# Performance work log

Hardware: AMD Instinct MI355X
Metric: run time of the kernel (lower is better)

The kernel has to match this reference:

```python
import jax, jax.numpy as jnp
import numpy as np

B, N, D, H = 4, 4096, 256, 8
HD = D // H
EPS = 1e-09


def _feature_map(t):
    # ELU(x) + 1, strictly positive feature map (Katharopoulos et al. 2020)
    return jax.nn.elu(t) + 1.0


def setup_inputs() -> dict:
    key = jax.random.key(0)
    ks = jax.random.split(key, 8)
    s = 0.02  # weight init scale for numerical stability
    return {
        "x": jax.random.normal(ks[0], (B, N, D), dtype=jnp.float32),
        "prior": jax.random.normal(ks[1], (B, N, N), dtype=jnp.float32),
        "Wq": jax.random.normal(ks[2], (D, D), dtype=jnp.float32) * s,
        "Wk": jax.random.normal(ks[3], (D, D), dtype=jnp.float32) * s,
        "Wv": jax.random.normal(ks[4], (D, D), dtype=jnp.float32) * s,
        "bv": jax.random.normal(ks[5], (D,), dtype=jnp.float32) * s,
        "Wo": jax.random.normal(ks[6], (D, D), dtype=jnp.float32) * s,
        "bo": jax.random.normal(ks[7], (D,), dtype=jnp.float32) * s,
    }


def reference(x, prior, Wq, Wk, Wv, bv, Wo, bo):
    b, n, d = x.shape
    # bias: mean over last axis of prior -> (b, n, 1, 1), broadcast over heads/dims
    bias = jnp.mean(prior, axis=-1)[:, :, None, None]
    q = _feature_map(jnp.einsum("bnd,ed->bne", x, Wq).reshape(b, n, H, HD) + bias)
    padding_mask = jnp.all(q == 0, axis=-1)  # (b, n, H)
    k = _feature_map(jnp.einsum("bnd,ed->bne", x, Wk).reshape(b, n, H, HD))
    v = _feature_map((jnp.einsum("bnd,ed->bne", x, Wv) + bv).reshape(b, n, H, HD))
    # KV summary state: (b, h, m, d) with m = value dim, d = key feature dim
    kv = jnp.einsum("bnhd,bnhm->bhmd", k, v)
    # normalizer: q . sum_n(k)
    z = 1.0 / (jnp.einsum("bnhd,bhd->bnh", q, jnp.sum(k, axis=1)) + EPS)
    attn = jnp.einsum("bnhd,bhmd,bnh->bnhm", q, kv, z)
    attn = jnp.where(padding_mask[..., None], 0.0, attn)
    attn = attn.reshape(b, n, H * HD)
    return jnp.einsum("bnd,ed->bne", attn, Wo) + bo
```

## Files before the change

kernel.cpp:

```cpp
#include <hip/hip_runtime.h>
#include <hip/hip_bf16.h>
#include <math.h>

#define B_ 4
#define N_ 4096
#define D_ 256
#define H_ 8
#define HD_ 32
#define TOKENS (B_ * N_)
#define EPSF 1e-9f
#define KV_CH 64

typedef __bf16 bf16x8 __attribute__((ext_vector_type(8)));
typedef float f32x4 __attribute__((ext_vector_type(4)));
typedef ushort ushort8_t __attribute__((ext_vector_type(8)));

__device__ __forceinline__ float elu1(float x) { return x > 0.f ? x + 1.f : __expf(x); }

__device__ __forceinline__ ushort f2bf(float f) {
    __hip_bfloat16 h = __float2bfloat16(f);
    return *reinterpret_cast<ushort*>(&h);
}

#define GLOAD_LDS16(g, l)                                                              \
    __builtin_amdgcn_global_load_lds((__attribute__((address_space(1))) const void*)(g), \
                                     (__attribute__((address_space(3))) void*)(l), 16, 0, 0)

#define MFMA16(a, b, c) __builtin_amdgcn_mfma_f32_16x16x32_bf16((a), (b), (c), 0, 0, 0)

__global__ __launch_bounds__(256) void k_cvt_w(const float* __restrict__ Wq,
                                               const float* __restrict__ Wk,
                                               const float* __restrict__ Wv,
                                               const float* __restrict__ Wo,
                                               ushort* __restrict__ dst) {
    const int i = blockIdx.x * 256 + threadIdx.x;
    const int sel = i >> 13;
    const float* src = sel == 0 ? Wq : sel == 1 ? Wk : sel == 2 ? Wv : Wo;
    const int j = i & 8191;
    const float4* s = (const float4*)src + (size_t)j * 2;
    const float4 a = s[0], b = s[1];
    ushort8_t o;
    o[0] = f2bf(a.x); o[1] = f2bf(a.y); o[2] = f2bf(a.z); o[3] = f2bf(a.w);
    o[4] = f2bf(b.x); o[5] = f2bf(b.y); o[6] = f2bf(b.z); o[7] = f2bf(b.w);
    *((ushort8_t*)dst + i) = o;
}

__global__ __launch_bounds__(512, 2) void k_mix2(const float* __restrict__ prior,
                                                 const float* __restrict__ x,
                                                 const ushort* __restrict__ wq,
                                                 const ushort* __restrict__ wk,
                                                 const ushort* __restrict__ wv,
                                                 const float* __restrict__ bv,
                                                 float* __restrict__ bias_g,
                                                 ushort* __restrict__ qpre,
                                                 ushort* __restrict__ kb,
                                                 ushort* __restrict__ vb) {
    __shared__ ushort As[32 * 256];
    __shared__ ushort Ws[3 * 256 * 32];
    const int t = threadIdx.x;
    const int w = t >> 6, lane = t & 63;
    const int bid = blockIdx.x;

    if (bid % 5 != 0) {
        const int bidx = bid - bid / 5 - 1;
        const int row = bidx * 8 + w;
        const f32x4* p = (const f32x4*)(prior + (size_t)row * N_);
        float s0 = 0.f, s1 = 0.f, s2 = 0.f, s3 = 0.f;
#pragma unroll
        for (int i = 0; i < 4; ++i) {
            const f32x4 a = __builtin_nontemporal_load(p + (i * 4 + 0) * 64 + lane);
            const f32x4 b = __builtin_nontemporal_load(p + (i * 4 + 1) * 64 + lane);
            const f32x4 c = __builtin_nontemporal_load(p + (i * 4 + 2) * 64 + lane);
            const f32x4 d = __builtin_nontemporal_load(p + (i * 4 + 3) * 64 + lane);
            s0 += a[0] + a[1] + a[2] + a[3];
            s1 += b[0] + b[1] + b[2] + b[3];
            s2 += c[0] + c[1] + c[2] + c[3];
            s3 += d[0] + d[1] + d[2] + d[3];
        }
        float s = (s0 + s1) + (s2 + s3);
#pragma unroll
        for (int off = 32; off; off >>= 1) s += __shfl_xor(s, off, 64);
        if (lane == 0) bias_g[row] = s * (1.0f / N_);
        return;
    }

    const int rowBase = (bid / 5) * 32;

    {
        const int r = t >> 4;
        const int c0 = (t & 15) * 4;
#pragma unroll
        for (int j = 0; j < 4; ++j) {
            const int c = c0 + j * 64;
            const float4 xv = *(const float4*)(x + (size_t)(rowBase + r) * 256 + c);
            ushort4 o;
            o.x = f2bf(xv.x); o.y = f2bf(xv.y); o.z = f2bf(xv.z); o.w = f2bf(xv.w);
            const int byte = (r * 512 + c * 2) ^ ((r & 7) << 4);
            *(ushort4*)((char*)As + byte) = o;
        }
    }

    const int wr = w >> 2, wc = w & 3;
    const int q_ = lane >> 4;
    f32x4 accq[4] = {}, acck[4] = {}, accv[4] = {};

    for (int kt = 0; kt < 256; kt += 32) {
        __syncthreads();
#pragma unroll
        for (int j = 0; j < 6; ++j) {
            const int c = j * 512 + t;
            const int idx = c & 1023;
            const int e = idx >> 2;
            const int pslot = idx & 3;
            const int qsrc = pslot ^ ((e >> 1) & 3);
            const ushort* srcm = (j < 2) ? wq : (j < 4) ? wk : wv;
            GLOAD_LDS16(srcm + (size_t)e * 256 + kt + qsrc * 8, (char*)Ws + c * 16);
        }
        __syncthreads();
        const int r = wr * 16 + (lane & 15);
        const int abyte = (r * 512 + (kt + q_ * 8) * 2) ^ ((r & 7) << 4);
        const bf16x8 af = *(const bf16x8*)((const char*)As + abyte);
#pragma unroll
        for (int n = 0; n < 4; ++n) {
            const int e = wc * 64 + n * 16 + (lane & 15);
            const int wbyte = e * 64 + ((q_ ^ ((e >> 1) & 3)) * 16);
            const bf16x8 bq = *(const bf16x8*)((const char*)Ws + wbyte);
            const bf16x8 bk = *(const bf16x8*)((const char*)Ws + 16384 + wbyte);
            const bf16x8 bw = *(const bf16x8*)((const char*)Ws + 32768 + wbyte);
            accq[n] = MFMA16(af, bq, accq[n]);
            acck[n] = MFMA16(af, bk, acck[n]);
            accv[n] = MFMA16(af, bw, accv[n]);
        }
    }

#pragma unroll
    for (int n = 0; n < 4; ++n)
#pragma unroll
        for (int j = 0; j < 4; ++j) {
            const int rl = wr * 16 + (lane >> 4) * 4 + j;
            const int col = wc * 64 + n * 16 + (lane & 15);
            const size_t go = (size_t)(rowBase + rl) * 256 + col;
            qpre[go] = f2bf(accq[n][j]);
            kb[go]   = f2bf(elu1(acck[n][j]));
            vb[go]   = f2bf(elu1(accv[n][j] + bv[col]));
        }
}

__global__ __launch_bounds__(256) void k_kvpart(const ushort* __restrict__ kmat,
                                                const ushort* __restrict__ vmat,
                                                float* __restrict__ part) {
    const int bh = blockIdx.x;
    const int b = bh >> 3, h = bh & 7;
    const int tok0 = b * N_ + blockIdx.y * 64;
    __shared__ float kt_[64][32];
    __shared__ float vt_[64][32];
    const int t = threadIdx.x;
    const int m = t >> 3;
    const int lvec = (t & 7) * 4;
#pragma unroll
    for (int half = 0; half < 2; ++half) {
        const int rr = (t >> 3) + half * 32;
        const size_t g = (size_t)(tok0 + rr) * D_ + h * HD_ + lvec;
        const ushort4 ku = *(const ushort4*)(kmat + g);
        const ushort4 vu = *(const ushort4*)(vmat + g);
        kt_[rr][lvec + 0] = __bfloat162float(*(const __hip_bfloat16*)&ku.x);
        kt_[rr][lvec + 1] = __bfloat162float(*(const __hip_bfloat16*)&ku.y);
        kt_[rr][lvec + 2] = __bfloat162float(*(const __hip_bfloat16*)&ku.z);
        kt_[rr][lvec + 3] = __bfloat162float(*(const __hip_bfloat16*)&ku.w);
        vt_[rr][lvec + 0] = __bfloat162float(*(const __hip_bfloat16*)&vu.x);
        vt_[rr][lvec + 1] = __bfloat162float(*(const __hip_bfloat16*)&vu.y);
        vt_[rr][lvec + 2] = __bfloat162float(*(const __hip_bfloat16*)&vu.z);
        vt_[rr][lvec + 3] = __bfloat162float(*(const __hip_bfloat16*)&vu.w);
    }
    __syncthreads();
    float4 acc = {0.f, 0.f, 0.f, 0.f};
    float4 sk = {0.f, 0.f, 0.f, 0.f};
#pragma unroll 4
    for (int r = 0; r < 64; ++r) {
        const float vv = vt_[r][m];
        const float4 kk = *(const float4*)&kt_[r][lvec];
        acc.x = fmaf(vv, kk.x, acc.x);
        acc.y = fmaf(vv, kk.y, acc.y);
        acc.z = fmaf(vv, kk.z, acc.z);
        acc.w = fmaf(vv, kk.w, acc.w);
        sk.x += kk.x; sk.y += kk.y; sk.z += kk.z; sk.w += kk.w;
    }
    float* outp = part + ((size_t)blockIdx.y * 32 + bh) * 1056;
    *(float4*)(outp + m * 32 + lvec) = acc;
    if (m == 0) *(float4*)(outp + 1024 + lvec) = sk;
}

__global__ __launch_bounds__(256) void k_kvred(const float* __restrict__ part,
                                               float* __restrict__ kv,
                                               float* __restrict__ ksum) {
    const int i = blockIdx.x * 256 + threadIdx.x;
    if (i >= 32 * 1056) return;
    const int bh = i / 1056, r = i - bh * 1056;
    float s = 0.f;
#pragma unroll 8
    for (int c = 0; c < KV_CH; ++c) s += part[((size_t)c * 32 + bh) * 1056 + r];
    if (r < 1024) kv[(size_t)bh * 1024 + r] = s;
    else          ksum[(size_t)bh * 32 + (r - 1024)] = s;
}

__global__ __launch_bounds__(512, 2) void k_fusedB(const ushort* __restrict__ qpre,
                                                   const float* __restrict__ bias_g,
                                                   const float* __restrict__ kv,
                                                   const float* __restrict__ ksum,
                                                   const ushort* __restrict__ wo,
                                                   const float* __restrict__ bo,
                                                   float* __restrict__ out) {
    __shared__ ushort qs[64 * 256];
    __shared__ ushort at_s[64 * 256];
    __shared__ ushort Ws2[256 * 32];
    const int t = threadIdx.x;
    const int w = t >> 6, lane = t & 63;
    const int tokBase = blockIdx.x * 64;
    const int b = tokBase >> 12;

#pragma unroll
    for (int j = 0; j < 4; ++j) {
        const int chunk = j * 512 + t;
        GLOAD_LDS16(qpre + (size_t)tokBase * 256 + (size_t)chunk * 8,
                    (char*)qs + chunk * 16);
    }

    const int c = t & 255;
    const int h = c >> 5, m = c & 31;
    f32x4 kvr[8], ksr[8];
#pragma unroll
    for (int i = 0; i < 8; ++i) {
        kvr[i] = *(const f32x4*)(kv + (((size_t)(b * H_ + h) * HD_ + m) * HD_) + i * 4);
        ksr[i] = *(const f32x4*)(ksum + (size_t)(b * H_ + h) * HD_ + i * 4);
    }
    __syncthreads();

    {
        const int r = t >> 3;
        const float brow = bias_g[tokBase + r];
        const int cb = (t & 7) * 32;
#pragma unroll
        for (int i = 0; i < 4; ++i) {
            bf16x8 qv = *(bf16x8*)(qs + r * 256 + cb + i * 8);
#pragma unroll
            for (int j = 0; j < 8; ++j) qv[j] = (__bf16)elu1((float)qv[j] + brow);
            *(bf16x8*)(qs + r * 256 + cb + i * 8) = qv;
        }
    }
    __syncthreads();

    for (int tok2 = 0; tok2 < 32; ++tok2) {
        const int tok = tok2 * 2 + (t >> 8);
        float num = 0.f, den = 0.f;
#pragma unroll
        for (int i = 0; i < 4; ++i) {
            const bf16x8 qv = *(const bf16x8*)(qs + tok * 256 + h * HD_ + i * 8);
#pragma unroll
            for (int j = 0; j < 8; ++j) {
                const float qf = (float)qv[j];
                num = fmaf(qf, ((const float*)kvr)[i * 8 + j], num);
                den = fmaf(qf, ((const float*)ksr)[i * 8 + j], den);
            }
        }
        const float a = num / (den + EPSF);
        const int byte = (tok * 512 + c * 2) ^ ((tok & 7) << 4);
        *(ushort*)((char*)at_s + byte) = f2bf(a);
    }

    const int wr = w >> 2, wc = w & 3;
    const int q_ = lane >> 4;
    f32x4 acc[2][4] = {};
    for (int kt = 0; kt < 256; kt += 32) {
        __syncthreads();
#pragma unroll
        for (int j = 0; j < 2; ++j) {
            const int ch = j * 512 + t;
            const int e = ch >> 2;
            const int pslot = ch & 3;
            const int qsrc = pslot ^ ((e >> 1) & 3);
            GLOAD_LDS16(wo + (size_t)e * 256 + kt + qsrc * 8, (char*)Ws2 + ch * 16);
        }
        __syncthreads();
        bf16x8 af[2];
#pragma unroll
        for (int mm = 0; mm < 2; ++mm) {
            const int r = wr * 32 + mm * 16 + (lane & 15);
            const int byte = (r * 512 + (kt + q_ * 8) * 2) ^ ((r & 7) << 4);
            af[mm] = *(const bf16x8*)((const char*)at_s + byte);
        }
#pragma unroll
        for (int n = 0; n < 4; ++n) {
            const int e = wc * 64 + n * 16 + (lane & 15);
            const int wbyte = e * 64 + ((q_ ^ ((e >> 1) & 3)) * 16);
            const bf16x8 bw = *(const bf16x8*)((const char*)Ws2 + wbyte);
#pragma unroll
            for (int mm = 0; mm < 2; ++mm)
                acc[mm][n] = MFMA16(af[mm], bw, acc[mm][n]);
        }
    }
#pragma unroll
    for (int mm = 0; mm < 2; ++mm)
#pragma unroll
        for (int n = 0; n < 4; ++n)
#pragma unroll
            for (int j = 0; j < 4; ++j) {
                const int row = tokBase + wr * 32 + mm * 16 + (lane >> 4) * 4 + j;
                const int col = wc * 64 + n * 16 + (lane & 15);
                out[(size_t)row * 256 + col] = acc[mm][n][j] + bo[col];
            }
}

extern "C" void kernel_launch(void* const* d_in, const int* in_sizes, int n_in,
                              void* d_out, int out_size, void* d_ws, size_t ws_size,
                              hipStream_t stream) {
    const float* x     = (const float*)d_in[0];
    const float* prior = (const float*)d_in[1];
    const float* Wq    = (const float*)d_in[2];
    const float* Wk    = (const float*)d_in[3];
    const float* Wv    = (const float*)d_in[4];
    const float* bv    = (const float*)d_in[5];
    const float* Wo    = (const float*)d_in[6];
    const float* bo    = (const float*)d_in[7];
    float* out = (float*)d_out;

    char* w8 = (char*)d_ws;
    ushort* qpre = (ushort*)w8;
    ushort* kb   = qpre + (size_t)TOKENS * D_;
    ushort* vb   = kb + (size_t)TOKENS * D_;
    ushort* wqb  = vb + (size_t)TOKENS * D_;
    ushort* wkb  = wqb + 65536;
    ushort* wvb  = wkb + 65536;
    ushort* wob  = wvb + 65536;
    float* kvb   = (float*)(wqb + 4 * 65536);
    float* ksb   = kvb + 32768;
    float* bias  = ksb + 1024;
    float* part  = bias + TOKENS;

    k_cvt_w<<<128, 256, 0, stream>>>(Wq, Wk, Wv, Wo, wqb);

    k_mix2<<<2560, 512, 0, stream>>>(prior, x, wqb, wkb, wvb, bv, bias, qpre, kb, vb);

    k_kvpart<<<dim3(32, KV_CH), 256, 0, stream>>>(kb, vb, part);
    k_kvred<<<132, 256, 0, stream>>>(part, kvb, ksb);

    k_fusedB<<<256, 512, 0, stream>>>(qpre, bias, kvb, ksb, wob, bo, out);
}
```

Measured before the change: 103.3 us.

## Fuse KV partial-sum computation into projection kernel using MFMA

The projection kernel no longer writes the K and V activations to global memory. It stages transposed K and V tiles in shared memory, reusing the weight buffer. There, each wave computes per-head 32-token KV outer-product partials and the key sums with bf16 MFMA, using a ones vector for the sums. This removes the separate k_kvpart launch and the global round trip of K and V. The reduction kernel now sums 128 partial chunks per batch instead of 64, which adds more partial-buffer traffic. Reusing Ws requires an extra barrier.

```diff
diff --git a/kernel.cpp b/kernel.cpp
--- a/kernel.cpp
+++ b/kernel.cpp
@@ -9,7 +9,6 @@
 #define HD_ 32
 #define TOKENS (B_ * N_)
 #define EPSF 1e-9f
-#define KV_CH 64
 
 typedef __bf16 bf16x8 __attribute__((ext_vector_type(8)));
 typedef float f32x4 __attribute__((ext_vector_type(4)));
@@ -53,8 +52,7 @@
                                                  const float* __restrict__ bv,
                                                  float* __restrict__ bias_g,
                                                  ushort* __restrict__ qpre,
-                                                 ushort* __restrict__ kb,
-                                                 ushort* __restrict__ vb) {
+                                                 float* __restrict__ part) {
     __shared__ ushort As[32 * 256];
     __shared__ ushort Ws[3 * 256 * 32];
     const int t = threadIdx.x;
@@ -84,7 +82,8 @@
         return;
     }
 
-    const int rowBase = (bid / 5) * 32;
+    const int qidx = bid / 5;
+    const int rowBase = qidx * 32;
 
     {
         const int r = t >> 4;
@@ -133,6 +132,10 @@
         }
     }
 
+    __syncthreads();
+
+    ushort* VT = Ws;
+    ushort* KT = Ws + 8192;
 #pragma unroll
     for (int n = 0; n < 4; ++n)
 #pragma unroll
@@ -141,53 +144,48 @@
             const int col = wc * 64 + n * 16 + (lane & 15);
             const size_t go = (size_t)(rowBase + rl) * 256 + col;
             qpre[go] = f2bf(accq[n][j]);
-            kb[go]   = f2bf(elu1(acck[n][j]));
-            vb[go]   = f2bf(elu1(accv[n][j] + bv[col]));
-        }
-}
-
-__global__ __launch_bounds__(256) void k_kvpart(const ushort* __restrict__ kmat,
-                                                const ushort* __restrict__ vmat,
-                                                float* __restrict__ part) {
-    const int bh = blockIdx.x;
-    const int b = bh >> 3, h = bh & 7;
-    const int tok0 = b * N_ + blockIdx.y * 64;
-    __shared__ float kt_[64][32];
-    __shared__ float vt_[64][32];
-    const int t = threadIdx.x;
-    const int m = t >> 3;
-    const int lvec = (t & 7) * 4;
-#pragma unroll
-    for (int half = 0; half < 2; ++half) {
-        const int rr = (t >> 3) + half * 32;
-        const size_t g = (size_t)(tok0 + rr) * D_ + h * HD_ + lvec;
-        const ushort4 ku = *(const ushort4*)(kmat + g);
-        const ushort4 vu = *(const ushort4*)(vmat + g);
-        kt_[rr][lvec + 0] = __bfloat162float(*(const __hip_bfloat16*)&ku.x);
-        kt_[rr][lvec + 1] = __bfloat162float(*(const __hip_bfloat16*)&ku.y);
-        kt_[rr][lvec + 2] = __bfloat162float(*(const __hip_bfloat16*)&ku.z);
-        kt_[rr][lvec + 3] = __bfloat162float(*(const __hip_bfloat16*)&ku.w);
-        vt_[rr][lvec + 0] = __bfloat162float(*(const __hip_bfloat16*)&vu.x);
-        vt_[rr][lvec + 1] = __bfloat162float(*(const __hip_bfloat16*)&vu.y);
-        vt_[rr][lvec + 2] = __bfloat162float(*(const __hip_bfloat16*)&vu.z);
-        vt_[rr][lvec + 3] = __bfloat162float(*(const __hip_bfloat16*)&vu.w);
-    }
+            const int head = col >> 5, dm = col & 31;
+            KT[head * 1024 + dm * 32 + rl] = f2bf(elu1(acck[n][j]));
+            VT[head * 1024 + dm * 32 + rl] = f2bf(elu1(accv[n][j] + bv[col]));
+        }
     __syncthreads();
-    float4 acc = {0.f, 0.f, 0.f, 0.f};
-    float4 sk = {0.f, 0.f, 0.f, 0.f};
-#pragma unroll 4
-    for (int r = 0; r < 64; ++r) {
-        const float vv = vt_[r][m];
-        const float4 kk = *(const float4*)&kt_[r][lvec];
-        acc.x = fmaf(vv, kk.x, acc.x);
-        acc.y = fmaf(vv, kk.y, acc.y);
-        acc.z = fmaf(vv, kk.z, acc.z);
-        acc.w = fmaf(vv, kk.w, acc.w);
-        sk.x += kk.x; sk.y += kk.y; sk.z += kk.z; sk.w += kk.w;
-    }
-    float* outp = part + ((size_t)blockIdx.y * 32 + bh) * 1056;
-    *(float4*)(outp + m * 32 + lvec) = acc;
-    if (m == 0) *(float4*)(outp + 1024 + lvec) = sk;
+
+    const ushort* vtw = VT + w * 1024;
+    const ushort* ktw = KT + w * 1024;
+    bf16x8 av[2], bk2[2];
+#pragma unroll
+    for (int i = 0; i < 2; ++i) {
+        av[i]  = *(const bf16x8*)(vtw + (i * 16 + (lane & 15)) * 32 + (lane >> 4) * 8);
+        bk2[i] = *(const bf16x8*)(ktw + (i * 16 + (lane & 15)) * 32 + (lane >> 4) * 8);
+    }
+    bf16x8 ones;
+#pragma unroll
+    for (int i = 0; i < 8; ++i) ones[i] = (__bf16)1.0f;
+    f32x4 kvacc[2][2] = {};
+    f32x4 ks[2] = {};
+#pragma unroll
+    for (int mi = 0; mi < 2; ++mi)
+#pragma unroll
+        for (int di = 0; di < 2; ++di)
+            kvacc[mi][di] = MFMA16(av[mi], bk2[di], kvacc[mi][di]);
+#pragma unroll
+    for (int di = 0; di < 2; ++di) ks[di] = MFMA16(ones, bk2[di], ks[di]);
+
+    float* pp = part + (size_t)qidx * 8448 + w * 1056;
+#pragma unroll
+    for (int mi = 0; mi < 2; ++mi)
+#pragma unroll
+        for (int di = 0; di < 2; ++di)
+#pragma unroll
+            for (int j = 0; j < 4; ++j) {
+                const int m = mi * 16 + (lane >> 4) * 4 + j;
+                const int d = di * 16 + (lane & 15);
+                pp[m * 32 + d] = kvacc[mi][di][j];
+            }
+    if ((lane >> 4) == 0) {
+        pp[1024 + (lane & 15)] = ks[0][0];
+        pp[1024 + 16 + (lane & 15)] = ks[1][0];
+    }
 }
 
 __global__ __launch_bounds__(256) void k_kvred(const float* __restrict__ part,
@@ -196,9 +194,11 @@
     const int i = blockIdx.x * 256 + threadIdx.x;
     if (i >= 32 * 1056) return;
     const int bh = i / 1056, r = i - bh * 1056;
+    const int b = bh >> 3, h = bh & 7;
     float s = 0.f;
 #pragma unroll 8
-    for (int c = 0; c < KV_CH; ++c) s += part[((size_t)c * 32 + bh) * 1056 + r];
+    for (int c = 0; c < 128; ++c)
+        s += part[(size_t)(b * 128 + c) * 8448 + h * 1056 + r];
     if (r < 1024) kv[(size_t)bh * 1024 + r] = s;
     else          ksum[(size_t)bh * 32 + (r - 1024)] = s;
 }
@@ -325,9 +325,7 @@
 
     char* w8 = (char*)d_ws;
     ushort* qpre = (ushort*)w8;
-    ushort* kb   = qpre + (size_t)TOKENS * D_;
-    ushort* vb   = kb + (size_t)TOKENS * D_;
-    ushort* wqb  = vb + (size_t)TOKENS * D_;
+    ushort* wqb  = qpre + (size_t)TOKENS * D_;
     ushort* wkb  = wqb + 65536;
     ushort* wvb  = wkb + 65536;
     ushort* wob  = wvb + 65536;
@@ -338,9 +336,8 @@
 
     k_cvt_w<<<128, 256, 0, stream>>>(Wq, Wk, Wv, Wo, wqb);
 
-    k_mix2<<<2560, 512, 0, stream>>>(prior, x, wqb, wkb, wvb, bv, bias, qpre, kb, vb);
-
-    k_kvpart<<<dim3(32, KV_CH), 256, 0, stream>>>(kb, vb, part);
+    k_mix2<<<2560, 512, 0, stream>>>(prior, x, wqb, wkb, wvb, bv, bias, qpre, part);
+
     k_kvred<<<132, 256, 0, stream>>>(part, kvb, ksb);
 
     k_fusedB<<<256, 512, 0, stream>>>(qpre, bias, kvb, ksb, wob, bo, out);
```

Result: faster. 96.29 us (-6.8%).
